# Optimization experiments

Hardware: AMD Instinct MI355X
Metric: run time of the kernel (lower is better)

## Reference

```python
import jax, jax.numpy as jnp
import numpy as np

IN_C = 512
OUT_C = 1024
N = 8192


def _xavier(key, shape):
    fan_in, fan_out = shape[1], shape[0]
    limit = float(np.sqrt(6.0 / (fan_in + fan_out)))
    return jax.random.uniform(key, shape, jnp.float32, -limit, limit)


def setup_inputs() -> dict:
    key = jax.random.key(0)
    ks = jax.random.split(key, 20)
    inp = {
        'x': jax.random.normal(ks[0], (IN_C, N), jnp.float32),
        'c_prev_dim0': jax.random.normal(ks[1], (OUT_C, N), jnp.float32),
        'h_prev_dim0': jax.random.normal(ks[2], (OUT_C, N), jnp.float32),
        'c_prev_dim1': jax.random.normal(ks[3], (OUT_C, N), jnp.float32),
        'h_prev_dim1': jax.random.normal(ks[4], (OUT_C, N), jnp.float32),
    }
    names_x = ['w_ii', 'w_if', 'w_ig', 'w_io']
    names_h = ['w_hi', 'w_hf', 'w_hg', 'w_ho']
    names_b = ['b_i', 'b_f', 'b_g', 'b_o']
    k = 5
    for n in names_x:
        inp[n] = _xavier(ks[k], (OUT_C, IN_C)); k += 1
    for n in names_h:
        inp[n] = _xavier(ks[k], (OUT_C, OUT_C)); k += 1
    for n in names_b:
        inp[n] = _xavier(ks[k], (OUT_C, 1)); k += 1
    inp['weighted_sum'] = jax.random.uniform(ks[k], (2,), jnp.float32)
    return inp


def reference(x, c_prev_dim0, h_prev_dim0, c_prev_dim1, h_prev_dim1,
              w_ii, w_if, w_ig, w_io,
              w_hi, w_hf, w_hg, w_ho,
              b_i, b_f, b_g, b_o,
              weighted_sum):
    # Input projections shared by both spatial directions: (out, N)
    xi = w_ii @ x
    xf = w_if @ x
    xg = w_ig @ x
    xo = w_io @ x

    def gates(h_prev, c_prev):
        i = jax.nn.sigmoid(xi + w_hi @ h_prev + b_i)
        f = jax.nn.sigmoid(xf + w_hf @ h_prev + b_f)
        g = jnp.tanh(xg + w_hg @ h_prev + b_g)
        o = jax.nn.sigmoid(xo + w_ho @ h_prev + b_o)
        c = f * c_prev + i * g
        h = o * jnp.tanh(c)
        return c, h

    ct0, ht0 = gates(h_prev_dim0, c_prev_dim0)
    ct1, ht1 = gates(h_prev_dim1, c_prev_dim1)
    ct = ct0 * weighted_sum[0] + ct1 * weighted_sum[1]
    ht = ht0 * weighted_sum[0] + ht1 * weighted_sum[1]
    return ct, ht
```

## Files before the change

kernel.cpp:

```cpp
#include <hip/hip_runtime.h>
#include <cstdint>
#include <cstddef>

#define IN_C  512
#define OUT_C 1024
#define NSAMP 8192

#define BM 64
#define BN 64
#define BK 64

typedef __bf16 bf16x8 __attribute__((ext_vector_type(8)));
typedef float  f32x4  __attribute__((ext_vector_type(4)));

__device__ __forceinline__ unsigned short f2bf(float f) {
    unsigned int u = __float_as_uint(f);
    u += 0x7FFFu + ((u >> 16) & 1u);
    return (unsigned short)(u >> 16);
}

__device__ __forceinline__ float sigmoid_f(float x) {
    return 1.0f / (1.0f + __expf(-x));
}
__device__ __forceinline__ float tanh_f(float x) {
    float e = __expf(2.0f * x);
    return 1.0f - 2.0f / (e + 1.0f);
}

__global__ void tcvt_kernel(const float* __restrict__ in, unsigned short* __restrict__ out,
                            int R, int C) {
    __shared__ float t[32][33];
    const int tx = threadIdx.x;
    const int ty = threadIdx.y;
    const int c0 = blockIdx.x * 32;
    const int r0 = blockIdx.y * 32;
#pragma unroll
    for (int i = 0; i < 4; ++i)
        t[ty + i * 8][tx] = in[(size_t)(r0 + ty + i * 8) * C + (c0 + tx)];
    __syncthreads();
#pragma unroll
    for (int i = 0; i < 4; ++i)
        out[(size_t)(c0 + ty + i * 8) * R + (r0 + tx)] = f2bf(t[tx][ty + i * 8]);
}

__global__ void cvt_kernel(const float* __restrict__ in, unsigned short* __restrict__ out, int n4) {
    int idx = blockIdx.x * blockDim.x + threadIdx.x;
    if (idx < n4) {
        float4 v = reinterpret_cast<const float4*>(in)[idx];
        ushort4 o;
        o.x = f2bf(v.x); o.y = f2bf(v.y); o.z = f2bf(v.z); o.w = f2bf(v.w);
        reinterpret_cast<ushort4*>(out)[idx] = o;
    }
}

__global__ __launch_bounds__(256, 2) void mdlstm_main(
    const unsigned short* __restrict__ xT,
    const unsigned short* __restrict__ h0T,
    const unsigned short* __restrict__ h1T,
    const unsigned short* __restrict__ wx,
    const unsigned short* __restrict__ wh,
    const float* __restrict__ b_i, const float* __restrict__ b_f,
    const float* __restrict__ b_g, const float* __restrict__ b_o,
    const float* __restrict__ cp0, const float* __restrict__ cp1,
    const float* __restrict__ wsum,
    float* __restrict__ out)
{
    __shared__ __align__(16) unsigned char smem[6 * 8192];

    const int tid  = threadIdx.x;
    const int lane = tid & 63;
    const int wid  = tid >> 6;
    const int wm   = wid >> 1;
    const int wn   = wid & 1;
    const int g4   = lane >> 4;
    const int l16  = lane & 15;

    const int brow = blockIdx.y * BM;
    const int bcol = blockIdx.x * BN;

    f32x4 acc[2][4][2][2];
#pragma unroll
    for (int d = 0; d < 2; ++d)
#pragma unroll
        for (int q = 0; q < 4; ++q)
#pragma unroll
            for (int a = 0; a < 2; ++a)
#pragma unroll
                for (int b = 0; b < 2; ++b)
                    acc[d][q][a][b] = (f32x4){0.f, 0.f, 0.f, 0.f};

    auto stage_tile = [&](const unsigned short* gbase, int pitch_bytes, int k0bytes, int lds_base) {
#pragma unroll
        for (int j = 0; j < 2; ++j) {
            const int slot = wid * 2 + j;
            const int u    = slot * 1024 + lane * 16;
            const int row  = u >> 7;
            const int kb   = u & 127;
            const char* src = (const char*)gbase + (size_t)row * pitch_bytes + k0bytes
                              + (kb ^ ((row & 7) << 4));
            __builtin_amdgcn_global_load_lds((const unsigned int*)src,
                                             (unsigned int*)(smem + lds_base + slot * 1024),
                                             16, 0, 0);
        }
    };

    auto frag_at = [&](int lds_base, int row, int kbyte) -> bf16x8 {
        const int off = lds_base + row * 128 + (kbyte ^ ((row & 7) << 4));
        return *reinterpret_cast<const bf16x8*>(smem + off);
    };

    for (int st = 0; st < IN_C / BK; ++st) {
        const int k0b = st * BK * 2;
#pragma unroll
        for (int q = 0; q < 4; ++q)
            stage_tile(wx + (size_t)q * OUT_C * IN_C + (size_t)brow * IN_C, IN_C * 2, k0b, q * 8192);
        stage_tile(xT + (size_t)bcol * IN_C, IN_C * 2, k0b, 4 * 8192);
        __syncthreads();
#pragma unroll
        for (int kk = 0; kk < 2; ++kk) {
            const int kbyte = kk * 64 + g4 * 16;
            bf16x8 afr[4][2], bfr[2];
#pragma unroll
            for (int q = 0; q < 4; ++q)
#pragma unroll
                for (int fm = 0; fm < 2; ++fm)
                    afr[q][fm] = frag_at(q * 8192, wm * 32 + fm * 16 + l16, kbyte);
#pragma unroll
            for (int fn = 0; fn < 2; ++fn)
                bfr[fn] = frag_at(4 * 8192, wn * 32 + fn * 16 + l16, kbyte);
#pragma unroll
            for (int q = 0; q < 4; ++q)
#pragma unroll
                for (int fm = 0; fm < 2; ++fm)
#pragma unroll
                    for (int fn = 0; fn < 2; ++fn)
                        acc[0][q][fm][fn] = __builtin_amdgcn_mfma_f32_16x16x32_bf16(
                            afr[q][fm], bfr[fn], acc[0][q][fm][fn], 0, 0, 0);
        }
        __syncthreads();
    }

#pragma unroll
    for (int q = 0; q < 4; ++q)
#pragma unroll
        for (int a = 0; a < 2; ++a)
#pragma unroll
            for (int b = 0; b < 2; ++b)
                acc[1][q][a][b] = acc[0][q][a][b];

    for (int st = 0; st < OUT_C / BK; ++st) {
        const int k0b = st * BK * 2;
#pragma unroll
        for (int q = 0; q < 4; ++q)
            stage_tile(wh + (size_t)q * OUT_C * OUT_C + (size_t)brow * OUT_C, OUT_C * 2, k0b, q * 8192);
        stage_tile(h0T + (size_t)bcol * OUT_C, OUT_C * 2, k0b, 4 * 8192);
        stage_tile(h1T + (size_t)bcol * OUT_C, OUT_C * 2, k0b, 5 * 8192);
        __syncthreads();
#pragma unroll
        for (int kk = 0; kk < 2; ++kk) {
            const int kbyte = kk * 64 + g4 * 16;
            bf16x8 afr[4][2], b0f[2], b1f[2];
#pragma unroll
            for (int q = 0; q < 4; ++q)
#pragma unroll
                for (int fm = 0; fm < 2; ++fm)
                    afr[q][fm] = frag_at(q * 8192, wm * 32 + fm * 16 + l16, kbyte);
#pragma unroll
            for (int fn = 0; fn < 2; ++fn) {
                b0f[fn] = frag_at(4 * 8192, wn * 32 + fn * 16 + l16, kbyte);
                b1f[fn] = frag_at(5 * 8192, wn * 32 + fn * 16 + l16, kbyte);
            }
#pragma unroll
            for (int q = 0; q < 4; ++q)
#pragma unroll
                for (int fm = 0; fm < 2; ++fm)
#pragma unroll
                    for (int fn = 0; fn < 2; ++fn) {
                        acc[0][q][fm][fn] = __builtin_amdgcn_mfma_f32_16x16x32_bf16(
                            afr[q][fm], b0f[fn], acc[0][q][fm][fn], 0, 0, 0);
                        acc[1][q][fm][fn] = __builtin_amdgcn_mfma_f32_16x16x32_bf16(
                            afr[q][fm], b1f[fn], acc[1][q][fm][fn], 0, 0, 0);
                    }
        }
        __syncthreads();
    }

    const float w0 = wsum[0], w1 = wsum[1];
#pragma unroll
    for (int fm = 0; fm < 2; ++fm)
#pragma unroll
        for (int fn = 0; fn < 2; ++fn)
#pragma unroll
            for (int r = 0; r < 4; ++r) {
                const int m = brow + wm * 32 + fm * 16 + g4 * 4 + r;
                const int n = bcol + wn * 32 + fn * 16 + l16;
                const size_t idx = (size_t)m * NSAMP + n;
                const float bi = b_i[m], bff = b_f[m], bg = b_g[m], bo = b_o[m];

                float c0v, h0v, c1v, h1v;
                {
                    float i_ = sigmoid_f(acc[0][0][fm][fn][r] + bi);
                    float f_ = sigmoid_f(acc[0][1][fm][fn][r] + bff);
                    float g_ = tanh_f   (acc[0][2][fm][fn][r] + bg);
                    float o_ = sigmoid_f(acc[0][3][fm][fn][r] + bo);
                    float c_ = f_ * cp0[idx] + i_ * g_;
                    c0v = c_;
                    h0v = o_ * tanh_f(c_);
                }
                {
                    float i_ = sigmoid_f(acc[1][0][fm][fn][r] + bi);
                    float f_ = sigmoid_f(acc[1][1][fm][fn][r] + bff);
                    float g_ = tanh_f   (acc[1][2][fm][fn][r] + bg);
                    float o_ = sigmoid_f(acc[1][3][fm][fn][r] + bo);
                    float c_ = f_ * cp1[idx] + i_ * g_;
                    c1v = c_;
                    h1v = o_ * tanh_f(c_);
                }
                out[idx] = w0 * c0v + w1 * c1v;
                out[(size_t)OUT_C * NSAMP + idx] = w0 * h0v + w1 * h1v;
            }
}

extern "C" void kernel_launch(void* const* d_in, const int* in_sizes, int n_in,
                              void* d_out, int out_size, void* d_ws, size_t ws_size,
                              hipStream_t stream) {
    (void)in_sizes; (void)n_in; (void)out_size; (void)ws_size;

    const float* x    = (const float*)d_in[0];
    const float* cp0  = (const float*)d_in[1];
    const float* hp0  = (const float*)d_in[2];
    const float* cp1  = (const float*)d_in[3];
    const float* hp1  = (const float*)d_in[4];
    const float* wxp[4] = {(const float*)d_in[5], (const float*)d_in[6],
                           (const float*)d_in[7], (const float*)d_in[8]};
    const float* whp[4] = {(const float*)d_in[9], (const float*)d_in[10],
                           (const float*)d_in[11], (const float*)d_in[12]};
    const float* b_i  = (const float*)d_in[13];
    const float* b_f  = (const float*)d_in[14];
    const float* b_g  = (const float*)d_in[15];
    const float* b_o  = (const float*)d_in[16];
    const float* wsum = (const float*)d_in[17];
    float* out = (float*)d_out;

    char* ws = (char*)d_ws;
    unsigned short* xT  = (unsigned short*)(ws);
    unsigned short* h0T = (unsigned short*)(ws + (size_t)8  * 1024 * 1024);
    unsigned short* h1T = (unsigned short*)(ws + (size_t)24 * 1024 * 1024);
    unsigned short* wxc = (unsigned short*)(ws + (size_t)40 * 1024 * 1024);
    unsigned short* whc = (unsigned short*)(ws + (size_t)44 * 1024 * 1024);

    dim3 tb(32, 8);
    tcvt_kernel<<<dim3(NSAMP / 32, IN_C  / 32), tb, 0, stream>>>(x,   xT,  IN_C,  NSAMP);
    tcvt_kernel<<<dim3(NSAMP / 32, OUT_C / 32), tb, 0, stream>>>(hp0, h0T, OUT_C, NSAMP);
    tcvt_kernel<<<dim3(NSAMP / 32, OUT_C / 32), tb, 0, stream>>>(hp1, h1T, OUT_C, NSAMP);

    for (int q = 0; q < 4; ++q)
        cvt_kernel<<<(OUT_C * IN_C / 4) / 256, 256, 0, stream>>>(
            wxp[q], wxc + (size_t)q * OUT_C * IN_C, OUT_C * IN_C / 4);
    for (int q = 0; q < 4; ++q)
        cvt_kernel<<<(OUT_C * OUT_C / 4) / 256, 256, 0, stream>>>(
            whp[q], whc + (size_t)q * OUT_C * OUT_C, OUT_C * OUT_C / 4);

    mdlstm_main<<<dim3(NSAMP / BN, OUT_C / BM), 256, 0, stream>>>(
        xT, h0T, h1T, wxc, whc, b_i, b_f, b_g, b_o, cp0, cp1, wsum, out);
}
```

Baseline: 250.2 us.

## Double-buffer LDS with async global-to-LDS prefetch and widen tile to 64x128

Replaces the synchronous stage-then-compute loop with a double-buffered pipeline in which the next K-slice is loaded into LDS with global_load_lds while MFMAs run on the current one. Phases are interleaved with manual vmcnt waits, raw s_barrier and setprio. The block grows to 512 threads covering 64x128 outputs, and the LDS layout changes to 64-byte half-K rows with a new XOR swizzle. The aim is to hide global memory latency and raise reuse of the weight tiles. The cost is 128KB of LDS per block, which limits occupancy, plus fragile hand-counted waits.

```diff
diff --git a/kernel.cpp b/kernel.cpp
--- a/kernel.cpp
+++ b/kernel.cpp
@@ -6,12 +6,11 @@
 #define OUT_C 1024
 #define NSAMP 8192
 
-#define BM 64
-#define BN 64
-#define BK 64
-
 typedef __bf16 bf16x8 __attribute__((ext_vector_type(8)));
 typedef float  f32x4  __attribute__((ext_vector_type(4)));
+
+#define VMCNT(N)  asm volatile("s_waitcnt vmcnt(" #N ")" ::: "memory")
+#define BARRIER() asm volatile("s_barrier" ::: "memory")
 
 __device__ __forceinline__ unsigned short f2bf(float f) {
     unsigned int u = __float_as_uint(f);
@@ -53,7 +52,27 @@
     }
 }
 
-__global__ __launch_bounds__(256, 2) void mdlstm_main(
+template<int G0, int G1, int ND>
+__device__ __forceinline__ void mfma_phase(f32x4 (&acc)[2][4][2][2],
+                                           const bf16x8 (&aF0)[2],
+                                           const bf16x8 (&aF1)[2],
+                                           const bf16x8 (&bF)[2][2]) {
+    __builtin_amdgcn_s_setprio(1);
+#pragma unroll
+    for (int d = 0; d < ND; ++d)
+#pragma unroll
+        for (int fm = 0; fm < 2; ++fm)
+#pragma unroll
+            for (int fn = 0; fn < 2; ++fn) {
+                acc[d][G0][fm][fn] = __builtin_amdgcn_mfma_f32_16x16x32_bf16(
+                    aF0[fm], bF[d][fn], acc[d][G0][fm][fn], 0, 0, 0);
+                acc[d][G1][fm][fn] = __builtin_amdgcn_mfma_f32_16x16x32_bf16(
+                    aF1[fm], bF[d][fn], acc[d][G1][fm][fn], 0, 0, 0);
+            }
+    __builtin_amdgcn_s_setprio(0);
+}
+
+__global__ __launch_bounds__(512, 2) void mdlstm_main(
     const unsigned short* __restrict__ xT,
     const unsigned short* __restrict__ h0T,
     const unsigned short* __restrict__ h1T,
@@ -65,18 +84,20 @@
     const float* __restrict__ wsum,
     float* __restrict__ out)
 {
-    __shared__ __align__(16) unsigned char smem[6 * 8192];
+    __shared__ __align__(16) unsigned char smem[131072];
 
     const int tid  = threadIdx.x;
     const int lane = tid & 63;
     const int wid  = tid >> 6;
-    const int wm   = wid >> 1;
-    const int wn   = wid & 1;
+    const int wm   = wid >> 2;
+    const int wn   = wid & 3;
     const int g4   = lane >> 4;
     const int l16  = lane & 15;
 
-    const int brow = blockIdx.y * BM;
-    const int bcol = blockIdx.x * BN;
+    const int brow = blockIdx.y * 64;
+    const int bcol = blockIdx.x * 128;
+
+    const int s_off16 = tid * 16;
 
     f32x4 acc[2][4][2][2];
 #pragma unroll
@@ -89,55 +110,96 @@
                 for (int b = 0; b < 2; ++b)
                     acc[d][q][a][b] = (f32x4){0.f, 0.f, 0.f, 0.f};
 
-    auto stage_tile = [&](const unsigned short* gbase, int pitch_bytes, int k0bytes, int lds_base) {
-#pragma unroll
-        for (int j = 0; j < 2; ++j) {
-            const int slot = wid * 2 + j;
-            const int u    = slot * 1024 + lane * 16;
-            const int row  = u >> 7;
-            const int kb   = u & 127;
-            const char* src = (const char*)gbase + (size_t)row * pitch_bytes + k0bytes
-                              + (kb ^ ((row & 7) << 4));
+    auto stage_A_half = [&](int buf, int h, const unsigned short* w, int pitchE, int k0) {
+#pragma unroll
+        for (int i = 0; i < 2; ++i) {
+            const int u   = i * 8192 + s_off16;
+            const int q   = u >> 12;
+            const int v   = u & 4095;
+            const int row = v >> 6;
+            const int kb  = v & 63;
+            const char* src = (const char*)w
+                + ((size_t)q * OUT_C * pitchE + (size_t)(brow + row) * pitchE + k0 + h * 32) * 2
+                + (kb ^ ((((row >> 1) & 3)) << 4));
             __builtin_amdgcn_global_load_lds((const unsigned int*)src,
-                                             (unsigned int*)(smem + lds_base + slot * 1024),
-                                             16, 0, 0);
+                (unsigned int*)(smem + buf * 65536 + h * 32768 + i * 8192 + s_off16), 16, 0, 0);
         }
     };
-
-    auto frag_at = [&](int lds_base, int row, int kbyte) -> bf16x8 {
-        const int off = lds_base + row * 128 + (kbyte ^ ((row & 7) << 4));
+    auto stage_B_half = [&](int buf, int h, int d, const unsigned short* hT, int pitchE, int k0) {
+        const int row = s_off16 >> 6;
+        const int kb  = s_off16 & 63;
+        const char* src = (const char*)hT
+            + ((size_t)(bcol + row) * pitchE + k0 + h * 32) * 2
+            + (kb ^ ((((row >> 1) & 3)) << 4));
+        __builtin_amdgcn_global_load_lds((const unsigned int*)src,
+            (unsigned int*)(smem + buf * 65536 + h * 32768 + 16384 + d * 8192 + s_off16), 16, 0, 0);
+    };
+
+    auto fragA = [&](int buf, int h, int q, int fm) -> bf16x8 {
+        const int row = wm * 32 + fm * 16 + l16;
+        const int off = buf * 65536 + h * 32768 + q * 4096 + row * 64
+                        + ((g4 * 16) ^ ((((row >> 1) & 3)) << 4));
         return *reinterpret_cast<const bf16x8*>(smem + off);
     };
-
-    for (int st = 0; st < IN_C / BK; ++st) {
-        const int k0b = st * BK * 2;
-#pragma unroll
-        for (int q = 0; q < 4; ++q)
-            stage_tile(wx + (size_t)q * OUT_C * IN_C + (size_t)brow * IN_C, IN_C * 2, k0b, q * 8192);
-        stage_tile(xT + (size_t)bcol * IN_C, IN_C * 2, k0b, 4 * 8192);
-        __syncthreads();
-#pragma unroll
-        for (int kk = 0; kk < 2; ++kk) {
-            const int kbyte = kk * 64 + g4 * 16;
-            bf16x8 afr[4][2], bfr[2];
-#pragma unroll
-            for (int q = 0; q < 4; ++q)
-#pragma unroll
-                for (int fm = 0; fm < 2; ++fm)
-                    afr[q][fm] = frag_at(q * 8192, wm * 32 + fm * 16 + l16, kbyte);
-#pragma unroll
-            for (int fn = 0; fn < 2; ++fn)
-                bfr[fn] = frag_at(4 * 8192, wn * 32 + fn * 16 + l16, kbyte);
-#pragma unroll
-            for (int q = 0; q < 4; ++q)
-#pragma unroll
-                for (int fm = 0; fm < 2; ++fm)
-#pragma unroll
-                    for (int fn = 0; fn < 2; ++fn)
-                        acc[0][q][fm][fn] = __builtin_amdgcn_mfma_f32_16x16x32_bf16(
-                            afr[q][fm], bfr[fn], acc[0][q][fm][fn], 0, 0, 0);
-        }
-        __syncthreads();
+    auto fragB = [&](int buf, int h, int d, int fn) -> bf16x8 {
+        const int row = wn * 32 + fn * 16 + l16;
+        const int off = buf * 65536 + h * 32768 + 16384 + d * 8192 + row * 64
+                        + ((g4 * 16) ^ ((((row >> 1) & 3)) << 4));
+        return *reinterpret_cast<const bf16x8*>(smem + off);
+    };
+
+    bf16x8 aF0[2], aF1[2];
+    bf16x8 bF[2][2];
+
+    stage_A_half(0, 0, wx, IN_C, 0);
+    stage_B_half(0, 0, 0, xT, IN_C, 0);
+    stage_A_half(0, 1, wx, IN_C, 0);
+    stage_B_half(0, 1, 0, xT, IN_C, 0);
+    VMCNT(3);
+    BARRIER();
+
+    for (int st = 0; st < 8; ++st) {
+        const int cur = st & 1, nxt = cur ^ 1;
+        const bool last = (st == 7);
+        const int k0n = last ? 0 : (st + 1) * 64;
+
+#pragma unroll
+        for (int fn = 0; fn < 2; ++fn) bF[0][fn] = fragB(cur, 0, 0, fn);
+#pragma unroll
+        for (int fm = 0; fm < 2; ++fm) { aF0[fm] = fragA(cur, 0, 0, fm); aF1[fm] = fragA(cur, 0, 1, fm); }
+        if (!last) stage_A_half(nxt, 0, wx, IN_C, k0n);
+        else       stage_A_half(nxt, 0, wh, OUT_C, 0);
+        BARRIER();
+        mfma_phase<0, 1, 1>(acc, aF0, aF1, bF);
+        BARRIER();
+
+#pragma unroll
+        for (int fm = 0; fm < 2; ++fm) { aF0[fm] = fragA(cur, 0, 2, fm); aF1[fm] = fragA(cur, 0, 3, fm); }
+        if (!last) { stage_B_half(nxt, 0, 0, xT, IN_C, k0n); }
+        else       { stage_B_half(nxt, 0, 0, h0T, OUT_C, 0); stage_B_half(nxt, 0, 1, h1T, OUT_C, 0); }
+        BARRIER();
+        mfma_phase<2, 3, 1>(acc, aF0, aF1, bF);
+        if (!last) { VMCNT(3); } else { VMCNT(4); }
+        BARRIER();
+
+#pragma unroll
+        for (int fn = 0; fn < 2; ++fn) bF[0][fn] = fragB(cur, 1, 0, fn);
+#pragma unroll
+        for (int fm = 0; fm < 2; ++fm) { aF0[fm] = fragA(cur, 1, 0, fm); aF1[fm] = fragA(cur, 1, 1, fm); }
+        if (!last) stage_A_half(nxt, 1, wx, IN_C, k0n);
+        else       stage_A_half(nxt, 1, wh, OUT_C, 0);
+        BARRIER();
+        mfma_phase<0, 1, 1>(acc, aF0, aF1, bF);
+        BARRIER();
+
+#pragma unroll
+        for (int fm = 0; fm < 2; ++fm) { aF0[fm] = fragA(cur, 1, 2, fm); aF1[fm] = fragA(cur, 1, 3, fm); }
+        if (!last) { stage_B_half(nxt, 1, 0, xT, IN_C, k0n); }
+        else       { stage_B_half(nxt, 1, 0, h0T, OUT_C, 0); stage_B_half(nxt, 1, 1, h1T, OUT_C, 0); }
+        BARRIER();
+        mfma_phase<2, 3, 1>(acc, aF0, aF1, bF);
+        if (!last) { VMCNT(3); } else { VMCNT(4); }
+        BARRIER();
     }
 
 #pragma unroll
@@ -148,41 +210,47 @@
             for (int b = 0; b < 2; ++b)
                 acc[1][q][a][b] = acc[0][q][a][b];
 
-    for (int st = 0; st < OUT_C / BK; ++st) {
-        const int k0b = st * BK * 2;
-#pragma unroll
-        for (int q = 0; q < 4; ++q)
-            stage_tile(wh + (size_t)q * OUT_C * OUT_C + (size_t)brow * OUT_C, OUT_C * 2, k0b, q * 8192);
-        stage_tile(h0T + (size_t)bcol * OUT_C, OUT_C * 2, k0b, 4 * 8192);
-        stage_tile(h1T + (size_t)bcol * OUT_C, OUT_C * 2, k0b, 5 * 8192);
-        __syncthreads();
-#pragma unroll
-        for (int kk = 0; kk < 2; ++kk) {
-            const int kbyte = kk * 64 + g4 * 16;
-            bf16x8 afr[4][2], b0f[2], b1f[2];
-#pragma unroll
-            for (int q = 0; q < 4; ++q)
-#pragma unroll
-                for (int fm = 0; fm < 2; ++fm)
-                    afr[q][fm] = frag_at(q * 8192, wm * 32 + fm * 16 + l16, kbyte);
-#pragma unroll
-            for (int fn = 0; fn < 2; ++fn) {
-                b0f[fn] = frag_at(4 * 8192, wn * 32 + fn * 16 + l16, kbyte);
-                b1f[fn] = frag_at(5 * 8192, wn * 32 + fn * 16 + l16, kbyte);
-            }
-#pragma unroll
-            for (int q = 0; q < 4; ++q)
-#pragma unroll
-                for (int fm = 0; fm < 2; ++fm)
-#pragma unroll
-                    for (int fn = 0; fn < 2; ++fn) {
-                        acc[0][q][fm][fn] = __builtin_amdgcn_mfma_f32_16x16x32_bf16(
-                            afr[q][fm], b0f[fn], acc[0][q][fm][fn], 0, 0, 0);
-                        acc[1][q][fm][fn] = __builtin_amdgcn_mfma_f32_16x16x32_bf16(
-                            afr[q][fm], b1f[fn], acc[1][q][fm][fn], 0, 0, 0);
-                    }
-        }
-        __syncthreads();
+    for (int st = 0; st < 16; ++st) {
+        const int cur = st & 1, nxt = cur ^ 1;
+        const bool last = (st == 15);
+        const int k0n = last ? 0 : (st + 1) * 64;
+
+#pragma unroll
+        for (int d = 0; d < 2; ++d)
+#pragma unroll
+            for (int fn = 0; fn < 2; ++fn) bF[d][fn] = fragB(cur, 0, d, fn);
+#pragma unroll
+        for (int fm = 0; fm < 2; ++fm) { aF0[fm] = fragA(cur, 0, 0, fm); aF1[fm] = fragA(cur, 0, 1, fm); }
+        if (!last) stage_A_half(nxt, 0, wh, OUT_C, k0n);
+        BARRIER();
+        mfma_phase<0, 1, 2>(acc, aF0, aF1, bF);
+        BARRIER();
+
+#pragma unroll
+        for (int fm = 0; fm < 2; ++fm) { aF0[fm] = fragA(cur, 0, 2, fm); aF1[fm] = fragA(cur, 0, 3, fm); }
+        if (!last) { stage_B_half(nxt, 0, 0, h0T, OUT_C, k0n); stage_B_half(nxt, 0, 1, h1T, OUT_C, k0n); }
+        BARRIER();
+        mfma_phase<2, 3, 2>(acc, aF0, aF1, bF);
+        if (!last) { VMCNT(4); } else { VMCNT(0); }
+        BARRIER();
+
+#pragma unroll
+        for (int d = 0; d < 2; ++d)
+#pragma unroll
+            for (int fn = 0; fn < 2; ++fn) bF[d][fn] = fragB(cur, 1, d, fn);
+#pragma unroll
+        for (int fm = 0; fm < 2; ++fm) { aF0[fm] = fragA(cur, 1, 0, fm); aF1[fm] = fragA(cur, 1, 1, fm); }
+        if (!last) stage_A_half(nxt, 1, wh, OUT_C, k0n);
+        BARRIER();
+        mfma_phase<0, 1, 2>(acc, aF0, aF1, bF);
+        BARRIER();
+
+#pragma unroll
+        for (int fm = 0; fm < 2; ++fm) { aF0[fm] = fragA(cur, 1, 2, fm); aF1[fm] = fragA(cur, 1, 3, fm); }
+        if (!last) { stage_B_half(nxt, 1, 0, h0T, OUT_C, k0n); stage_B_half(nxt, 1, 1, h1T, OUT_C, k0n); }
+        BARRIER();
+        mfma_phase<2, 3, 2>(acc, aF0, aF1, bF);
+        if (!last) { VMCNT(4); BARRIER(); }
     }
 
     const float w0 = wsum[0], w1 = wsum[1];
@@ -261,6 +329,6 @@
         cvt_kernel<<<(OUT_C * OUT_C / 4) / 256, 256, 0, stream>>>(
             whp[q], whc + (size_t)q * OUT_C * OUT_C, OUT_C * OUT_C / 4);
 
-    mdlstm_main<<<dim3(NSAMP / BN, OUT_C / BM), 256, 0, stream>>>(
+    mdlstm_main<<<dim3(NSAMP / 128, OUT_C / 64), 512, 0, stream>>>(
         xT, h0T, h1T, wxc, whc, b_i, b_f, b_g, b_o, cp0, cp1, wsum, out);
 }
```

Result: no change. 247.6 us (-1.0%).
